# Kernel optimization log

Hardware: AMD Instinct MI355X
Metric: run time of the kernel (lower is better)

Reference implementation:

```python
import jax, jax.numpy as jnp
import numpy as np

N = 100000   # nodes
E = 500000   # edges
NS = 64      # scalar (0e) multiplicity
NV = 32      # vector (1o) multiplicity
DIM = NS + 3 * NV  # 160
AVG_NEI = 5.0
INV_SQRT3 = 0.5773502691896258


def setup_inputs() -> dict:
    key = jax.random.key(0)
    ks = jax.random.split(key, 14)
    return {
        "node_feats": jax.random.normal(ks[0], (N, DIM), jnp.float32),
        "node_attrs": jax.random.normal(ks[1], (N, 4), jnp.float32),
        "edge_message": jax.random.normal(ks[2], (E, DIM), jnp.float32),
        "edge_index": jax.random.randint(ks[3], (2, E), 0, N, dtype=jnp.int32),
        # UVU tensor product internal shared weights (one weight per u channel per path)
        "w_tp_00": jax.random.normal(ks[4], (NS,), jnp.float32),  # 0e x 0e -> 0e
        "w_tp_01": jax.random.normal(ks[5], (NS,), jnp.float32),  # 0e x 1o -> 1o
        "w_tp_10": jax.random.normal(ks[6], (NV,), jnp.float32),  # 1o x 0e -> 1o
        "w_tp_11": jax.random.normal(ks[7], (NV,), jnp.float32),  # 1o x 1o -> 0e
        # irreps Linear: tp out has 96x0e + 96x1o -> 96x0e + 32x1o
        "W_lin_s": jax.random.normal(ks[8], (NS + NV, NS + NV), jnp.float32),
        "W_lin_v": jax.random.normal(ks[9], (NS + NV, NV), jnp.float32),
        # FullyConnectedTensorProduct self-connection (uvw, v=1)
        "W_sc_000": jax.random.normal(ks[10], (NS, NS + NV), jnp.float32),
        "W_sc_110": jax.random.normal(ks[11], (NV, NS + NV), jnp.float32),
        "W_sc_011": jax.random.normal(ks[12], (NS, NV), jnp.float32),
        "W_sc_101": jax.random.normal(ks[13], (NV, NV), jnp.float32),
    }


def reference(node_feats, node_attrs, edge_message, edge_index,
              w_tp_00, w_tp_01, w_tp_10, w_tp_11,
              W_lin_s, W_lin_v, W_sc_000, W_sc_110, W_sc_011, W_sc_101):
    edge_dst = edge_index[1]
    # scatter-aggregate edge messages per destination node
    msg = jax.ops.segment_sum(edge_message, edge_dst, num_segments=N)
    msg = msg / jnp.sqrt(AVG_NEI)

    ms = msg[:, :NS]                         # [N, 64] scalars
    mv = msg[:, NS:].reshape(N, NV, 3)       # [N, 32, 3] vectors
    a_s = node_attrs[:, :1]                  # [N, 1]
    a_v = node_attrs[:, 1:]                  # [N, 3]

    # UVU tensor product (msg x attrs), per-channel shared weights
    s00 = ms * a_s * w_tp_00                                            # [N,64] 0e
    s11 = jnp.einsum('nuc,nc->nu', mv, a_v) * INV_SQRT3 * w_tp_11       # [N,32] 0e
    v01 = ms[:, :, None] * a_v[:, None, :] * w_tp_01[None, :, None]     # [N,64,3] 1o
    v10 = mv * a_s[:, :, None] * w_tp_10[None, :, None]                 # [N,32,3] 1o
    tp_s = jnp.concatenate([s00, s11], axis=1)   # [N,96]
    tp_v = jnp.concatenate([v01, v10], axis=1)   # [N,96,3]

    # irreps Linear (block diagonal per l, fan-in normalized)
    inv_fan = 1.0 / jnp.sqrt(jnp.float32(NS + NV))
    lin_s = (tp_s @ W_lin_s) * inv_fan                              # [N,96]
    lin_v = jnp.einsum('nuc,uw->nwc', tp_v, W_lin_v) * inv_fan      # [N,32,3]

    # self-connection: FullyConnectedTensorProduct(node_feats_in, node_attrs)
    xs = node_feats[:, :NS]
    xv = node_feats[:, NS:].reshape(N, NV, 3)
    inv2 = 1.0 / jnp.sqrt(2.0)
    sc_s = ((xs * a_s) @ W_sc_000 / jnp.sqrt(jnp.float32(NS))
            + (jnp.einsum('nuc,nc->nu', xv, a_v) * INV_SQRT3) @ W_sc_110 / jnp.sqrt(jnp.float32(NV))) * inv2
    sc_v = (jnp.einsum('nu,uw,nc->nwc', xs, W_sc_011, a_v) / jnp.sqrt(jnp.float32(NS))
            + jnp.einsum('nuc,uw->nwc', xv * a_s[:, :, None], W_sc_101) / jnp.sqrt(jnp.float32(NV))) * inv2

    h_s = lin_s + sc_s   # [N,96] = 64 scalars + 32 gates
    h_v = lin_v + sc_v   # [N,32,3]

    # gated activation: silu on scalars, sigmoid gates scale the vectors
    out_s = jax.nn.silu(h_s[:, :NS])
    gates = jax.nn.sigmoid(h_s[:, NS:])
    out_v = gates[:, :, None] * h_v
    return jnp.concatenate([out_s, out_v.reshape(N, NV * 3)], axis=1)  # [N,160]
```

## Files before the change

kernel.cpp:

```cpp
#include <hip/hip_runtime.h>

typedef unsigned short u16;
typedef unsigned int u32;

#define Nn 100000
#define Ee 500000
#define DIM 160
#define CAP 48

__device__ __forceinline__ float bf2f(u16 u) {
    return __uint_as_float(((u32)u) << 16);
}
__device__ __forceinline__ u16 f2bf(float f) {
    u32 i = __float_as_uint(f);
    return (u16)((i + 0x7FFFu + ((i >> 16) & 1u)) >> 16);
}

__global__ __launch_bounds__(256) void hist_fill_k(const int* __restrict__ ei,
                                                   int* __restrict__ cnt,
                                                   int* __restrict__ bucket) {
    int e = blockIdx.x * 256 + threadIdx.x;
    if (e >= Ee) return;
    int dst = ei[Ee + e];
    int pos = atomicAdd(&cnt[dst], 1);
    if (pos < CAP) bucket[(size_t)dst * CAP + pos] = e;
}

__global__ __launch_bounds__(256) void gather_k(const float* __restrict__ em,
                                                const int* __restrict__ bucket,
                                                const int* __restrict__ cnt,
                                                float* __restrict__ msg) {
    int gid = blockIdx.x * 256 + threadIdx.x;
    int n = gid >> 6;
    int lane = gid & 63;
    if (n >= Nn) return;
    int deg = cnt[n];
    if (deg > CAP) deg = CAP;
    const int* base = bucket + (size_t)n * CAP;
    float a0 = 0.f, a1 = 0.f, a2 = 0.f;
    for (int i = 0; i < deg; ++i) {
        int e = base[i];
        const float* r = em + (size_t)e * DIM;
        a0 += r[lane];
        a1 += r[64 + lane];
        if (lane < 32) a2 += r[128 + lane];
    }
    const float s = 0.4472135954999579f;
    float* q = msg + (size_t)n * DIM;
    q[lane] = a0 * s;
    q[64 + lane] = a1 * s;
    if (lane < 32) q[128 + lane] = a2 * s;
}

__global__ void transpose_f2b_k(const float* __restrict__ in, u16* __restrict__ outp) {
    __shared__ float t[32][33];
    int r0 = blockIdx.x * 32, c0 = blockIdx.y * 32;
    int tx = threadIdx.x, ty = threadIdx.y;
    t[ty][tx] = in[(size_t)(r0 + ty) * DIM + c0 + tx];
    __syncthreads();
    outp[(size_t)(c0 + ty) * Nn + r0 + tx] = f2bf(t[tx][ty]);
}

__global__ __launch_bounds__(256) void prep_weights_k(
    const float* __restrict__ Wls, const float* __restrict__ Wlv,
    const float* __restrict__ W000, const float* __restrict__ W110,
    const float* __restrict__ W011, const float* __restrict__ W101,
    const float* __restrict__ w00, const float* __restrict__ w01,
    const float* __restrict__ w10, const float* __restrict__ w11,
    float* __restrict__ W) {
    int i = blockIdx.x * 256 + threadIdx.x;
    const float inv_fan = 0.10206207261596577f;
    const float IS3 = 0.5773502691896258f;
    if (i < 9216) {
        int u = i / 96;
        float sc = inv_fan * (u < 64 ? w00[u] : IS3 * w11[u - 64]);
        W[i] = Wls[i] * sc;
    } else if (i < 12288) {
        int j = i - 9216; int u = j / 32;
        float sc = inv_fan * (u < 64 ? w01[u] : w10[u - 64]);
        W[i] = Wlv[j] * sc;
    } else if (i < 18432) {
        W[i] = W000[i - 12288] * 0.08838834764831845f;
    } else if (i < 21504) {
        W[i] = W110[i - 18432] * (0.125f * IS3);
    } else if (i < 23552) {
        W[i] = W011[i - 21504] * 0.08838834764831845f;
    } else {
        W[i] = W101[i - 23552] * 0.125f;
    }
}

__global__ __launch_bounds__(256) void node_k(
    const u16* __restrict__ msgT,
    const u16* __restrict__ featsT,
    const float* __restrict__ attrs,
    const float* __restrict__ W,
    float* __restrict__ out)
{
    int n = blockIdx.x * 256 + threadIdx.x;
    bool active = (n < Nn);
    if (!active) n = Nn - 1;

    const float* Wls = W;
    const float* Wlv = W + 9216;
    const float* W000 = W + 12288;
    const float* W110 = W + 18432;
    const float* W011 = W + 21504;
    const float* W101 = W + 23552;

    float a_s, av[3];
    {
        float4 a = *reinterpret_cast<const float4*>(attrs + (size_t)n * 4);
        a_s = a.x; av[0] = a.y; av[1] = a.z; av[2] = a.w;
    }

    float sg[32];

    for (int wb = 0; wb < 3; ++wb) {
        float acc[32];
        #pragma unroll
        for (int w = 0; w < 32; ++w) acc[w] = 0.f;
        const float* R1 = Wls + wb * 32;
        const float* R2 = W000 + wb * 32;
        const float* R3 = W110 + wb * 32;
        for (int u = 0; u < 64; ++u) {
            float msa = bf2f(msgT[(size_t)u * Nn + n]) * a_s;
            float xsa = bf2f(featsT[(size_t)u * Nn + n]) * a_s;
            const float* r1 = R1 + u * 96;
            const float* r2 = R2 + u * 96;
            #pragma unroll
            for (int w = 0; w < 32; ++w) acc[w] += msa * r1[w] + xsa * r2[w];
        }
        for (int j = 0; j < 32; ++j) {
            size_t d = (size_t)(64 + 3 * j) * Nn + n;
            float dv = bf2f(msgT[d]) * av[0] + bf2f(msgT[d + Nn]) * av[1]
                     + bf2f(msgT[d + 2 * Nn]) * av[2];
            float dx = bf2f(featsT[d]) * av[0] + bf2f(featsT[d + Nn]) * av[1]
                     + bf2f(featsT[d + 2 * Nn]) * av[2];
            const float* r1 = R1 + (64 + j) * 96;
            const float* r2 = R3 + j * 96;
            #pragma unroll
            for (int w = 0; w < 32; ++w) acc[w] += dv * r1[w] + dx * r2[w];
        }
        if (wb < 2) {
            #pragma unroll
            for (int w = 0; w < 32; ++w) {
                float h = acc[w];
                float o = h / (1.f + __expf(-h));
                if (active) out[(size_t)n * DIM + wb * 32 + w] = o;
            }
        } else {
            #pragma unroll
            for (int w = 0; w < 32; ++w) sg[w] = 1.f / (1.f + __expf(-acc[w]));
        }
    }

    float ss[32];
    #pragma unroll
    for (int w = 0; w < 32; ++w) ss[w] = 0.f;
    for (int u = 0; u < 64; ++u) {
        float m = bf2f(msgT[(size_t)u * Nn + n]);
        float x = bf2f(featsT[(size_t)u * Nn + n]);
        const float* r1 = Wlv + u * 32;
        const float* r2 = W011 + u * 32;
        #pragma unroll
        for (int w = 0; w < 32; ++w) ss[w] += m * r1[w] + x * r2[w];
    }

    #pragma unroll
    for (int c = 0; c < 3; ++c) {
        float hv[32];
        #pragma unroll
        for (int w = 0; w < 32; ++w) hv[w] = av[c] * ss[w];
        for (int j = 0; j < 32; ++j) {
            size_t d = (size_t)(64 + 3 * j + c) * Nn + n;
            float m = bf2f(msgT[d]) * a_s;
            float x = bf2f(featsT[d]) * a_s;
            const float* r1 = Wlv + (64 + j) * 32;
            const float* r2 = W101 + j * 32;
            #pragma unroll
            for (int w = 0; w < 32; ++w) hv[w] += m * r1[w] + x * r2[w];
        }
        if (active) {
            #pragma unroll
            for (int w = 0; w < 32; ++w)
                out[(size_t)n * DIM + 64 + 3 * w + c] = sg[w] * hv[w];
        }
    }
}

extern "C" void kernel_launch(void* const* d_in, const int* in_sizes, int n_in,
                              void* d_out, int out_size, void* d_ws, size_t ws_size,
                              hipStream_t stream) {
    const float* feats = (const float*)d_in[0];
    const float* attrs = (const float*)d_in[1];
    const float* em    = (const float*)d_in[2];
    const int*   ei    = (const int*)d_in[3];
    const float* w00   = (const float*)d_in[4];
    const float* w01   = (const float*)d_in[5];
    const float* w10   = (const float*)d_in[6];
    const float* w11   = (const float*)d_in[7];
    const float* Wls   = (const float*)d_in[8];
    const float* Wlv   = (const float*)d_in[9];
    const float* W000  = (const float*)d_in[10];
    const float* W110  = (const float*)d_in[11];
    const float* W011  = (const float*)d_in[12];
    const float* W101  = (const float*)d_in[13];

    char* ws = (char*)d_ws;
    int*   bucket = (int*)  (ws);
    int*   cnt    = (int*)  (ws + 19200000);
    float* msg    = (float*)(ws + 19600000);
    u16*   msgT   = (u16*)  (ws + 83600000);
    u16*   featsT = (u16*)  (ws + 115600000);
    float* W      = (float*)(ws + 147600000);

    hipMemsetAsync(cnt, 0, Nn * sizeof(int), stream);

    hist_fill_k<<<(Ee + 255) / 256, 256, 0, stream>>>(ei, cnt, bucket);

    gather_k<<<(Nn * 64 + 255) / 256, 256, 0, stream>>>(em, bucket, cnt, msg);

    dim3 tb(32, 32);
    transpose_f2b_k<<<dim3(Nn / 32, DIM / 32), tb, 0, stream>>>(msg, msgT);
    transpose_f2b_k<<<dim3(Nn / 32, DIM / 32), tb, 0, stream>>>(feats, featsT);

    prep_weights_k<<<96, 256, 0, stream>>>(Wls, Wlv, W000, W110, W011, W101,
                                           w00, w01, w10, w11, W);

    node_k<<<(Nn + 255) / 256, 256, 0, stream>>>(msgT, featsT, attrs, W, (float*)d_out);
}
```

Before: 885.2 us.

## Fuse gather with bf16 transpose and split node kernel across output blocks

The edge gather now writes bf16 transposed messages directly through a shared-memory tile, which removes the fp32 msg buffer and one transpose pass. The monolithic per-node kernel is split into a scalar kernel, with a grid dimension over three 32-wide output blocks that writes gates to a buffer, and a vector kernel split over two 16-channel halves. Output stores are staged through shared memory so they coalesce. This adds parallelism and lowers register pressure, at the cost of reading the inputs several times and an extra gate buffer round trip.

```diff
diff --git a/kernel.cpp b/kernel.cpp
--- a/kernel.cpp
+++ b/kernel.cpp
@@ -26,30 +26,42 @@
     if (pos < CAP) bucket[(size_t)dst * CAP + pos] = e;
 }
 
-__global__ __launch_bounds__(256) void gather_k(const float* __restrict__ em,
-                                                const int* __restrict__ bucket,
-                                                const int* __restrict__ cnt,
-                                                float* __restrict__ msg) {
-    int gid = blockIdx.x * 256 + threadIdx.x;
-    int n = gid >> 6;
-    int lane = gid & 63;
-    if (n >= Nn) return;
-    int deg = cnt[n];
-    if (deg > CAP) deg = CAP;
-    const int* base = bucket + (size_t)n * CAP;
-    float a0 = 0.f, a1 = 0.f, a2 = 0.f;
-    for (int i = 0; i < deg; ++i) {
-        int e = base[i];
-        const float* r = em + (size_t)e * DIM;
-        a0 += r[lane];
-        a1 += r[64 + lane];
-        if (lane < 32) a2 += r[128 + lane];
-    }
+__global__ __launch_bounds__(256) void gather_tr_k(const float* __restrict__ em,
+                                                   const int* __restrict__ bucket,
+                                                   const int* __restrict__ cnt,
+                                                   u16* __restrict__ msgT) {
+    __shared__ u16 tile[160][66];
+    int n0 = blockIdx.x * 64;
+    int w = threadIdx.x >> 6;
+    int lane = threadIdx.x & 63;
     const float s = 0.4472135954999579f;
-    float* q = msg + (size_t)n * DIM;
-    q[lane] = a0 * s;
-    q[64 + lane] = a1 * s;
-    if (lane < 32) q[128 + lane] = a2 * s;
+
+    for (int i = 0; i < 16; ++i) {
+        int n = n0 + w * 16 + i;
+        float a0 = 0.f, a1 = 0.f, a2 = 0.f;
+        if (n < Nn) {
+            int deg = cnt[n];
+            if (deg > CAP) deg = CAP;
+            const int* base = bucket + (size_t)n * CAP;
+            for (int k = 0; k < deg; ++k) {
+                int e = base[k];
+                const float* r = em + (size_t)e * DIM;
+                a0 += r[lane];
+                a1 += r[64 + lane];
+                if (lane < 32) a2 += r[128 + lane];
+            }
+        }
+        int col = w * 16 + i;
+        tile[lane][col] = f2bf(a0 * s);
+        tile[64 + lane][col] = f2bf(a1 * s);
+        if (lane < 32) tile[128 + lane][col] = f2bf(a2 * s);
+    }
+    __syncthreads();
+    for (int k = 0; k < 40; ++k) {
+        int d = w * 40 + k;
+        int n = n0 + lane;
+        if (n < Nn) msgT[(size_t)d * Nn + n] = tile[d][lane];
+    }
 }
 
 __global__ void transpose_f2b_k(const float* __restrict__ in, u16* __restrict__ outp) {
@@ -90,102 +102,146 @@
     }
 }
 
-__global__ __launch_bounds__(256) void node_k(
-    const u16* __restrict__ msgT,
-    const u16* __restrict__ featsT,
-    const float* __restrict__ attrs,
-    const float* __restrict__ W,
-    float* __restrict__ out)
-{
-    int n = blockIdx.x * 256 + threadIdx.x;
+__global__ __launch_bounds__(256) void node_s_k(
+    const u16* __restrict__ msgT, const u16* __restrict__ featsT,
+    const float* __restrict__ attrs, const float* __restrict__ W,
+    float* __restrict__ out, float* __restrict__ gbuf) {
+    __shared__ float st[256][33];
+    int wb = blockIdx.y;
+    int n0 = blockIdx.x * 256;
+    int t = threadIdx.x;
+    int n = n0 + t;
     bool active = (n < Nn);
-    if (!active) n = Nn - 1;
-
-    const float* Wls = W;
-    const float* Wlv = W + 9216;
+    int nc = active ? n : (Nn - 1);
+
+    const float* Wls  = W;
     const float* W000 = W + 12288;
     const float* W110 = W + 18432;
+
+    float4 a = *reinterpret_cast<const float4*>(attrs + (size_t)nc * 4);
+    float a_s = a.x, av0 = a.y, av1 = a.z, av2 = a.w;
+
+    float accU[32], accJ[32];
+    #pragma unroll
+    for (int w = 0; w < 32; ++w) { accU[w] = 0.f; accJ[w] = 0.f; }
+
+    const float* R1 = Wls + wb * 32;
+    const float* R2 = W000 + wb * 32;
+    const float* R3 = W110 + wb * 32;
+
+    for (int u = 0; u < 64; ++u) {
+        float m = bf2f(msgT[(size_t)u * Nn + nc]);
+        float x = bf2f(featsT[(size_t)u * Nn + nc]);
+        const float* r1 = R1 + u * 96;
+        const float* r2 = R2 + u * 96;
+        #pragma unroll
+        for (int w = 0; w < 32; ++w) accU[w] += m * r1[w] + x * r2[w];
+    }
+    for (int j = 0; j < 32; ++j) {
+        size_t d = (size_t)(64 + 3 * j) * Nn + nc;
+        float dv = bf2f(msgT[d]) * av0 + bf2f(msgT[d + Nn]) * av1
+                 + bf2f(msgT[d + 2 * Nn]) * av2;
+        float dx = bf2f(featsT[d]) * av0 + bf2f(featsT[d + Nn]) * av1
+                 + bf2f(featsT[d + 2 * Nn]) * av2;
+        const float* r1 = R1 + (64 + j) * 96;
+        const float* r2 = R3 + j * 96;
+        #pragma unroll
+        for (int w = 0; w < 32; ++w) accJ[w] += dv * r1[w] + dx * r2[w];
+    }
+
+    if (wb < 2) {
+        #pragma unroll
+        for (int w = 0; w < 32; ++w) {
+            float h = a_s * accU[w] + accJ[w];
+            st[t][w] = h / (1.f + __expf(-h));
+        }
+        __syncthreads();
+        int off = wb * 32;
+        for (int k = 0; k < 32; ++k) {
+            int f = k * 256 + t;
+            int node = f >> 5, w = f & 31;
+            int n2 = n0 + node;
+            if (n2 < Nn) out[(size_t)n2 * DIM + off + w] = st[node][w];
+        }
+    } else {
+        #pragma unroll
+        for (int w = 0; w < 32; ++w) {
+            float h = a_s * accU[w] + accJ[w];
+            if (active) gbuf[(size_t)w * Nn + n] = 1.f / (1.f + __expf(-h));
+        }
+    }
+}
+
+__global__ __launch_bounds__(256) void node_v_k(
+    const u16* __restrict__ msgT, const u16* __restrict__ featsT,
+    const float* __restrict__ attrs, const float* __restrict__ W,
+    const float* __restrict__ gbuf, float* __restrict__ out) {
+    __shared__ float st[256][49];
+    int half = blockIdx.y;
+    int w0 = half * 16;
+    int n0 = blockIdx.x * 256;
+    int t = threadIdx.x;
+    int n = n0 + t;
+    bool active = (n < Nn);
+    int nc = active ? n : (Nn - 1);
+
+    const float* Wlv  = W + 9216;
     const float* W011 = W + 21504;
     const float* W101 = W + 23552;
 
-    float a_s, av[3];
-    {
-        float4 a = *reinterpret_cast<const float4*>(attrs + (size_t)n * 4);
-        a_s = a.x; av[0] = a.y; av[1] = a.z; av[2] = a.w;
-    }
-
-    float sg[32];
-
-    for (int wb = 0; wb < 3; ++wb) {
-        float acc[32];
-        #pragma unroll
-        for (int w = 0; w < 32; ++w) acc[w] = 0.f;
-        const float* R1 = Wls + wb * 32;
-        const float* R2 = W000 + wb * 32;
-        const float* R3 = W110 + wb * 32;
-        for (int u = 0; u < 64; ++u) {
-            float msa = bf2f(msgT[(size_t)u * Nn + n]) * a_s;
-            float xsa = bf2f(featsT[(size_t)u * Nn + n]) * a_s;
-            const float* r1 = R1 + u * 96;
-            const float* r2 = R2 + u * 96;
-            #pragma unroll
-            for (int w = 0; w < 32; ++w) acc[w] += msa * r1[w] + xsa * r2[w];
-        }
-        for (int j = 0; j < 32; ++j) {
-            size_t d = (size_t)(64 + 3 * j) * Nn + n;
-            float dv = bf2f(msgT[d]) * av[0] + bf2f(msgT[d + Nn]) * av[1]
-                     + bf2f(msgT[d + 2 * Nn]) * av[2];
-            float dx = bf2f(featsT[d]) * av[0] + bf2f(featsT[d + Nn]) * av[1]
-                     + bf2f(featsT[d + 2 * Nn]) * av[2];
-            const float* r1 = R1 + (64 + j) * 96;
-            const float* r2 = R3 + j * 96;
-            #pragma unroll
-            for (int w = 0; w < 32; ++w) acc[w] += dv * r1[w] + dx * r2[w];
-        }
-        if (wb < 2) {
-            #pragma unroll
-            for (int w = 0; w < 32; ++w) {
-                float h = acc[w];
-                float o = h / (1.f + __expf(-h));
-                if (active) out[(size_t)n * DIM + wb * 32 + w] = o;
-            }
-        } else {
-            #pragma unroll
-            for (int w = 0; w < 32; ++w) sg[w] = 1.f / (1.f + __expf(-acc[w]));
-        }
-    }
-
-    float ss[32];
-    #pragma unroll
-    for (int w = 0; w < 32; ++w) ss[w] = 0.f;
+    float4 a = *reinterpret_cast<const float4*>(attrs + (size_t)nc * 4);
+    float a_s = a.x;
+    float av[3] = {a.y, a.z, a.w};
+
+    float ss[16];
+    #pragma unroll
+    for (int w = 0; w < 16; ++w) ss[w] = 0.f;
     for (int u = 0; u < 64; ++u) {
-        float m = bf2f(msgT[(size_t)u * Nn + n]);
-        float x = bf2f(featsT[(size_t)u * Nn + n]);
-        const float* r1 = Wlv + u * 32;
-        const float* r2 = W011 + u * 32;
-        #pragma unroll
-        for (int w = 0; w < 32; ++w) ss[w] += m * r1[w] + x * r2[w];
-    }
-
-    #pragma unroll
-    for (int c = 0; c < 3; ++c) {
-        float hv[32];
-        #pragma unroll
-        for (int w = 0; w < 32; ++w) hv[w] = av[c] * ss[w];
-        for (int j = 0; j < 32; ++j) {
-            size_t d = (size_t)(64 + 3 * j + c) * Nn + n;
-            float m = bf2f(msgT[d]) * a_s;
-            float x = bf2f(featsT[d]) * a_s;
-            const float* r1 = Wlv + (64 + j) * 32;
-            const float* r2 = W101 + j * 32;
-            #pragma unroll
-            for (int w = 0; w < 32; ++w) hv[w] += m * r1[w] + x * r2[w];
-        }
-        if (active) {
-            #pragma unroll
-            for (int w = 0; w < 32; ++w)
-                out[(size_t)n * DIM + 64 + 3 * w + c] = sg[w] * hv[w];
-        }
+        float m = bf2f(msgT[(size_t)u * Nn + nc]);
+        float x = bf2f(featsT[(size_t)u * Nn + nc]);
+        const float* r1 = Wlv + u * 32 + w0;
+        const float* r2 = W011 + u * 32 + w0;
+        #pragma unroll
+        for (int w = 0; w < 16; ++w) ss[w] += m * r1[w] + x * r2[w];
+    }
+
+    float hj[16][3];
+    #pragma unroll
+    for (int w = 0; w < 16; ++w) {
+        hj[w][0] = 0.f; hj[w][1] = 0.f; hj[w][2] = 0.f;
+    }
+    for (int j = 0; j < 32; ++j) {
+        size_t d = (size_t)(64 + 3 * j) * Nn + nc;
+        float m0 = bf2f(msgT[d]), m1 = bf2f(msgT[d + Nn]), m2 = bf2f(msgT[d + 2 * Nn]);
+        float x0 = bf2f(featsT[d]), x1 = bf2f(featsT[d + Nn]), x2 = bf2f(featsT[d + 2 * Nn]);
+        const float* r1 = Wlv + (64 + j) * 32 + w0;
+        const float* r2 = W101 + j * 32 + w0;
+        #pragma unroll
+        for (int w = 0; w < 16; ++w) {
+            float wv = r1[w], wx = r2[w];
+            hj[w][0] += m0 * wv + x0 * wx;
+            hj[w][1] += m1 * wv + x1 * wx;
+            hj[w][2] += m2 * wv + x2 * wx;
+        }
+    }
+
+    #pragma unroll
+    for (int w = 0; w < 16; ++w) {
+        float g = gbuf[(size_t)(w0 + w) * Nn + nc];
+        #pragma unroll
+        for (int c = 0; c < 3; ++c) {
+            float hv = av[c] * ss[w] + a_s * hj[w][c];
+            st[t][w * 3 + c] = g * hv;
+        }
+    }
+    __syncthreads();
+    int off = 64 + w0 * 3;
+    for (int k = 0; k < 48; ++k) {
+        int f = k * 256 + t;
+        int node = f / 48;
+        int idx = f - node * 48;
+        int n2 = n0 + node;
+        if (n2 < Nn) out[(size_t)n2 * DIM + off + idx] = st[node][idx];
     }
 }
 
@@ -210,23 +266,26 @@
     char* ws = (char*)d_ws;
     int*   bucket = (int*)  (ws);
     int*   cnt    = (int*)  (ws + 19200000);
-    float* msg    = (float*)(ws + 19600000);
-    u16*   msgT   = (u16*)  (ws + 83600000);
-    u16*   featsT = (u16*)  (ws + 115600000);
-    float* W      = (float*)(ws + 147600000);
+    u16*   msgT   = (u16*)  (ws + 19600000);
+    u16*   featsT = (u16*)  (ws + 51600000);
+    float* gbuf   = (float*)(ws + 83600000);
+    float* W      = (float*)(ws + 96400000);
 
     hipMemsetAsync(cnt, 0, Nn * sizeof(int), stream);
 
     hist_fill_k<<<(Ee + 255) / 256, 256, 0, stream>>>(ei, cnt, bucket);
 
-    gather_k<<<(Nn * 64 + 255) / 256, 256, 0, stream>>>(em, bucket, cnt, msg);
+    gather_tr_k<<<(Nn + 63) / 64, 256, 0, stream>>>(em, bucket, cnt, msgT);
 
     dim3 tb(32, 32);
-    transpose_f2b_k<<<dim3(Nn / 32, DIM / 32), tb, 0, stream>>>(msg, msgT);
     transpose_f2b_k<<<dim3(Nn / 32, DIM / 32), tb, 0, stream>>>(feats, featsT);
 
     prep_weights_k<<<96, 256, 0, stream>>>(Wls, Wlv, W000, W110, W011, W101,
                                            w00, w01, w10, w11, W);
 
-    node_k<<<(Nn + 255) / 256, 256, 0, stream>>>(msgT, featsT, attrs, W, (float*)d_out);
-}
+    node_s_k<<<dim3((Nn + 255) / 256, 3), 256, 0, stream>>>(msgT, featsT, attrs, W,
+                                                            (float*)d_out, gbuf);
+
+    node_v_k<<<dim3((Nn + 255) / 256, 2), 256, 0, stream>>>(msgT, featsT, attrs, W,
+                                                            gbuf, (float*)d_out);
+}
```

New measurement: 782.3 us. 1.13x faster.
